# Optimization experiments

Hardware: AMD Instinct MI355X
Metric: run time of the kernel (lower is better)

## Reference

```python
import jax, jax.numpy as jnp
import numpy as np

N = 10000
E = 320000
IN_DIM = 256
OUT_DIM = 64
ALPHA = 0.2          # LeakyReLU negative slope
NEG_FILL = -9e15     # mask value used by the original module


def setup_inputs() -> dict:
    key = jax.random.key(0)
    k1, k2, k3, k4, k5 = jax.random.split(key, 5)
    X = jax.random.normal(k1, (N, IN_DIM), dtype=jnp.float32)
    edges = jnp.stack([
        jax.random.randint(k2, (E,), 0, N, dtype=jnp.int64 if jax.config.jax_enable_x64 else jnp.int32),
        jax.random.randint(k3, (E,), 0, N, dtype=jnp.int64 if jax.config.jax_enable_x64 else jnp.int32),
    ], axis=0)
    # Xavier-uniform-like init scales (gain 1.414)
    wlim = 1.414 * np.sqrt(6.0 / (IN_DIM + OUT_DIM))
    alim = 1.414 * np.sqrt(6.0 / (2 * OUT_DIM + 1))
    W = jax.random.uniform(k4, (IN_DIM, OUT_DIM), minval=-wlim, maxval=wlim, dtype=jnp.float32)
    a = jax.random.uniform(k5, (2 * OUT_DIM, 1), minval=-alim, maxval=alim, dtype=jnp.float32)
    return {"X": X, "edges": edges, "W": W, "a": a}


def reference(X, edges, W, a):
    # dropout p=0.0 -> identity in both dropout layers
    Wh = X @ W                                   # [N, F_out]
    src, dst = edges[0], edges[1]
    # per-edge attention logit: leakyrelu([Wh_src || Wh_dst] @ a)
    # split a to avoid materializing the concatenated [E, 2F] tensor
    a_src, a_dst = a[:OUT_DIM, 0], a[OUT_DIM:, 0]
    e = (Wh @ a_src)[src] + (Wh @ a_dst)[dst]    # [E]
    e = jnp.where(e > 0, e, ALPHA * e)           # LeakyReLU
    # dense N x N masked attention, exactly as the original module
    att = jnp.full((N, N), NEG_FILL, dtype=Wh.dtype)
    att = att.at[src, dst].set(e)
    att = jax.nn.softmax(att, axis=1)            # row-wise softmax
    h_prime = att @ Wh                           # [N, F_out]
    return h_prime
```

## Files before the change

### kernel.cpp

```cpp
#include <hip/hip_runtime.h>

#define N_NODES 10000
#define IN_DIM  256
#define OUT_DIM 64
#define ALPHA   0.2f
#define CAPS    128
#define NBG     625

typedef __attribute__((ext_vector_type(8))) short short8v;
typedef __attribute__((ext_vector_type(4))) float f32x4;

__device__ __forceinline__ ushort f2bf(float f) {
    unsigned u = __float_as_uint(f);
    return (ushort)((u + 0x7FFFu + ((u >> 16) & 1u)) >> 16);
}
__device__ __forceinline__ float bf2f(ushort u) {
    return __uint_as_float((unsigned)u << 16);
}

__global__ __launch_bounds__(256) void k_prep(const float* __restrict__ W,
                                              int* __restrict__ cur,
                                              ushort* __restrict__ Wf) {
    const int gid = blockIdx.x * 256 + threadIdx.x;
    for (int i = gid; i < N_NODES; i += 10240) cur[i] = 0;
    for (int w = gid; w < IN_DIM * OUT_DIM; w += 10240) {
        int k = w >> 6, c = w & 63;
        int s = k >> 5, k5 = k & 31, g = k5 >> 3, j = k5 & 7;
        int ct = c >> 4, li = c & 15;
        Wf[(((s * 4 + ct) * 64) + (g * 16 + li)) * 8 + j] = f2bf(W[w]);
    }
}

__global__ __launch_bounds__(256) void k_fused(const float* __restrict__ X,
                                               const ushort* __restrict__ Wf,
                                               const float* __restrict__ a,
                                               const int* __restrict__ src,
                                               const int* __restrict__ dst,
                                               int E,
                                               ushort* __restrict__ Whb,
                                               float* __restrict__ es,
                                               float* __restrict__ ed,
                                               int* __restrict__ cur,
                                               int* __restrict__ slots) {
    const int t = threadIdx.x;
    const int b = blockIdx.x;

    if (b >= NBG) {
        int i0 = (b - NBG) * 512 + t;
#pragma unroll
        for (int u = 0; u < 2; ++u) {
            int i = i0 + u * 256;
            if (i < E) {
                int s = src[i], d = dst[i];
                int p = atomicAdd(&cur[s], 1);
                if (p < CAPS) slots[(size_t)s * CAPS + p] = d;
            }
        }
        return;
    }

    __shared__ float les[16], led[16];
    if (t < 16) { les[t] = 0.f; led[t] = 0.f; }
    __syncthreads();

    const int wave = t >> 6;
    const int lane = t & 63;
    const int g = lane >> 4, li = lane & 15;
    const int row0 = b * 16;
    const float* __restrict__ xrow = X + (size_t)(row0 + li) * IN_DIM + g * 8;
    const short8v* __restrict__ Wfrag = (const short8v*)Wf;

    f32x4 acc = {0.f, 0.f, 0.f, 0.f};
#pragma unroll
    for (int s = 0; s < 8; ++s) {
        float4 xa = *(const float4*)(xrow + s * 32);
        float4 xb = *(const float4*)(xrow + s * 32 + 4);
        short8v af;
        af[0] = (short)f2bf(xa.x); af[1] = (short)f2bf(xa.y);
        af[2] = (short)f2bf(xa.z); af[3] = (short)f2bf(xa.w);
        af[4] = (short)f2bf(xb.x); af[5] = (short)f2bf(xb.y);
        af[6] = (short)f2bf(xb.z); af[7] = (short)f2bf(xb.w);
        short8v bfv = Wfrag[(s * 4 + wave) * 64 + lane];
        acc = __builtin_amdgcn_mfma_f32_16x16x32_bf16(af, bfv, acc, 0, 0, 0);
    }

    const int colC = wave * 16 + li;
    const float asrc = a[colC];
    const float adst = a[OUT_DIM + colC];
#pragma unroll
    for (int j = 0; j < 4; ++j) {
        int row = row0 + g * 4 + j;
        float v = acc[j];
        Whb[(size_t)row * OUT_DIM + colC] = f2bf(v);
        float se = v * asrc, sd = v * adst;
        se += __shfl_xor(se, 1, 64); sd += __shfl_xor(sd, 1, 64);
        se += __shfl_xor(se, 2, 64); sd += __shfl_xor(sd, 2, 64);
        se += __shfl_xor(se, 4, 64); sd += __shfl_xor(sd, 4, 64);
        se += __shfl_xor(se, 8, 64); sd += __shfl_xor(sd, 8, 64);
        if (li == 0) {
            atomicAdd(&les[g * 4 + j], se);
            atomicAdd(&led[g * 4 + j], sd);
        }
    }
    __syncthreads();
    if (t < 16) { es[row0 + t] = les[t]; ed[row0 + t] = led[t]; }
}

__global__ __launch_bounds__(64) void k_attn_slots(const int* __restrict__ cur,
                                                   const int* __restrict__ slots,
                                                   const float* __restrict__ es,
                                                   const float* __restrict__ ed,
                                                   const ushort* __restrict__ Whb,
                                                   float* __restrict__ out) {
    const int r = blockIdx.x;
    const int lane = threadIdx.x;
    int deg = cur[r];
    if (deg > CAPS) deg = CAPS;

    if (deg == 0) {
        float acc = 0.f;
        for (int j = 0; j < N_NODES; ++j) acc += bf2f(Whb[(size_t)j * OUT_DIM + lane]);
        out[(size_t)r * OUT_DIM + lane] = acc / (float)N_NODES;
        return;
    }

    __shared__ int   htab[256];
    __shared__ int   sdst[CAPS];
    __shared__ float sp[CAPS];

    for (int i = lane; i < 256; i += 64) htab[i] = -1;
    __syncthreads();

    const float er = es[r];

    float m = -INFINITY;
    for (int i = lane; i < deg; i += 64) {
        int d = slots[(size_t)r * CAPS + i];
        float e = er + ed[d];
        e = e > 0.f ? e : ALPHA * e;
        bool first = true;
        unsigned h = ((unsigned)d * 2654435761u) >> 24;
        while (true) {
            int prev = atomicCAS(&htab[h], -1, d);
            if (prev == -1) break;
            if (prev == d) { first = false; break; }
            h = (h + 1) & 255;
        }
        if (!first) e = -INFINITY;
        sdst[i] = d;
        sp[i] = e;
        m = fmaxf(m, e);
    }
#pragma unroll
    for (int o = 32; o > 0; o >>= 1) m = fmaxf(m, __shfl_xor(m, o, 64));
    __syncthreads();

    float ssum = 0.f;
    for (int i = lane; i < deg; i += 64) {
        float p = __expf(sp[i] - m);
        sp[i] = p;
        ssum += p;
    }
#pragma unroll
    for (int o = 32; o > 0; o >>= 1) ssum += __shfl_xor(ssum, o, 64);
    __syncthreads();

    const int h2 = lane >> 5;
    const int c  = lane & 31;
    const ushort2* __restrict__ W2 = (const ushort2*)Whb;
    float ax = 0.f, ay = 0.f;
    const int npairs = deg >> 1;
    int ip = 0;
    for (; ip + 8 <= npairs; ip += 8) {
        float p[8]; int q[8]; ushort2 w[8];
#pragma unroll
        for (int u = 0; u < 8; ++u) {
            int i = 2 * (ip + u) + h2;
            p[u] = sp[i]; q[u] = sdst[i];
        }
#pragma unroll
        for (int u = 0; u < 8; ++u) w[u] = W2[(size_t)q[u] * 32 + c];
#pragma unroll
        for (int u = 0; u < 8; ++u) {
            ax = fmaf(p[u], bf2f(w[u].x), ax);
            ay = fmaf(p[u], bf2f(w[u].y), ay);
        }
    }
    for (; ip < npairs; ++ip) {
        int i = 2 * ip + h2;
        float p = sp[i];
        ushort2 w = W2[(size_t)sdst[i] * 32 + c];
        ax = fmaf(p, bf2f(w.x), ax);
        ay = fmaf(p, bf2f(w.y), ay);
    }
    if ((deg & 1) && h2 == 0) {
        int i = deg - 1;
        float p = sp[i];
        ushort2 w = W2[(size_t)sdst[i] * 32 + c];
        ax = fmaf(p, bf2f(w.x), ax);
        ay = fmaf(p, bf2f(w.y), ay);
    }
    ax += __shfl_xor(ax, 32, 64);
    ay += __shfl_xor(ay, 32, 64);
    if (h2 == 0) {
        float inv = 1.f / ssum;
        ((float2*)out)[(size_t)r * 32 + c] = make_float2(ax * inv, ay * inv);
    }
}

__global__ __launch_bounds__(256) void k_gemm_mfma(const float* __restrict__ X,
                                                   const float* __restrict__ W,
                                                   const float* __restrict__ a,
                                                   ushort* __restrict__ Whb,
                                                   float* __restrict__ es,
                                                   float* __restrict__ ed,
                                                   int* __restrict__ zero10k) {
    const int t = threadIdx.x;
    const int b = blockIdx.x;
    const int gid = b * 256 + t;
    if (gid < N_NODES) zero10k[gid] = 0;

    __shared__ short8v bfragv[8 * 4 * 64];
    __shared__ float les[16], led[16];
    for (int w = t; w < IN_DIM * OUT_DIM; w += 256) {
        int k = w >> 6, c = w & 63;
        int s = k >> 5, k5 = k & 31, g = k5 >> 3, j = k5 & 7;
        int ct = c >> 4, li = c & 15;
        ((ushort*)bfragv)[(((s * 4 + ct) * 64) + (g * 16 + li)) * 8 + j] = f2bf(W[w]);
    }
    if (t < 16) { les[t] = 0.f; led[t] = 0.f; }
    __syncthreads();

    const int wave = t >> 6, lane = t & 63;
    const int g = lane >> 4, li = lane & 15;
    const int row0 = b * 16;
    const float* __restrict__ xrow = X + (size_t)(row0 + li) * IN_DIM + g * 8;

    f32x4 acc = {0.f, 0.f, 0.f, 0.f};
#pragma unroll
    for (int s = 0; s < 8; ++s) {
        float4 xa = *(const float4*)(xrow + s * 32);
        float4 xb = *(const float4*)(xrow + s * 32 + 4);
        short8v af;
        af[0] = (short)f2bf(xa.x); af[1] = (short)f2bf(xa.y);
        af[2] = (short)f2bf(xa.z); af[3] = (short)f2bf(xa.w);
        af[4] = (short)f2bf(xb.x); af[5] = (short)f2bf(xb.y);
        af[6] = (short)f2bf(xb.z); af[7] = (short)f2bf(xb.w);
        short8v bfv = bfragv[(s * 4 + wave) * 64 + lane];
        acc = __builtin_amdgcn_mfma_f32_16x16x32_bf16(af, bfv, acc, 0, 0, 0);
    }
    const int colC = wave * 16 + li;
    const float asrc = a[colC];
    const float adst = a[OUT_DIM + colC];
#pragma unroll
    for (int j = 0; j < 4; ++j) {
        int row = row0 + g * 4 + j;
        float v = acc[j];
        Whb[(size_t)row * OUT_DIM + colC] = f2bf(v);
        float se = v * asrc, sd = v * adst;
        se += __shfl_xor(se, 1, 64); sd += __shfl_xor(sd, 1, 64);
        se += __shfl_xor(se, 2, 64); sd += __shfl_xor(sd, 2, 64);
        se += __shfl_xor(se, 4, 64); sd += __shfl_xor(sd, 4, 64);
        se += __shfl_xor(se, 8, 64); sd += __shfl_xor(sd, 8, 64);
        if (li == 0) { atomicAdd(&les[g * 4 + j], se); atomicAdd(&led[g * 4 + j], sd); }
    }
    __syncthreads();
    if (t < 16) { es[row0 + t] = les[t]; ed[row0 + t] = led[t]; }
}

__global__ void k_fill_slots(const int* __restrict__ src, const int* __restrict__ dst,
                             int E, int* __restrict__ cur, int* __restrict__ slots) {
    int i = blockIdx.x * 256 + threadIdx.x;
    if (i < E) {
        int s = src[i], d = dst[i];
        int p = atomicAdd(&cur[s], 1);
        if (p < CAPS) slots[(size_t)s * CAPS + p] = d;
    }
}

extern "C" void kernel_launch(void* const* d_in, const int* in_sizes, int n_in,
                              void* d_out, int out_size, void* d_ws, size_t ws_size,
                              hipStream_t stream) {
    const float* X     = (const float*)d_in[0];
    const int*   edges = (const int*)d_in[1];
    const float* W     = (const float*)d_in[2];
    const float* a     = (const float*)d_in[3];
    float* out = (float*)d_out;

    const int E = in_sizes[1] / 2;
    const int* src = edges;
    const int* dst = edges + E;

    char* ws = (char*)d_ws;
    size_t o = 0;
    auto carve = [&](size_t bytes) -> void* {
        o = (o + 255) & ~(size_t)255;
        void* p = ws + o;
        o += bytes;
        return p;
    };
    ushort* Whb   = (ushort*)carve((size_t)N_NODES * OUT_DIM * 2);
    float*  es    = (float*)carve((size_t)N_NODES * 4);
    float*  ed    = (float*)carve((size_t)N_NODES * 4);
    int*    cur   = (int*)carve((size_t)N_NODES * 4);
    int*    slots = (int*)carve((size_t)N_NODES * CAPS * 4);
    ushort* Wf    = (ushort*)carve((size_t)IN_DIM * OUT_DIM * 2);

    const int nsc = (E + 511) / 512;

    if (o <= ws_size) {
        k_prep      <<<40, 256, 0, stream>>>(W, cur, Wf);
        k_fused     <<<NBG + nsc, 256, 0, stream>>>(X, Wf, a, src, dst, E,
                                                    Whb, es, ed, cur, slots);
        k_attn_slots<<<N_NODES, 64, 0, stream>>>(cur, slots, es, ed, Whb, out);
    } else {
        k_gemm_mfma <<<NBG, 256, 0, stream>>>(X, W, a, Whb, es, ed, cur);
        k_fill_slots<<<(E + 255) / 256, 256, 0, stream>>>(src, dst, E, cur, slots);
        k_attn_slots<<<N_NODES, 64, 0, stream>>>(cur, slots, es, ed, Whb, out);
    }
}
```

Measured before the change: 44.78 us.

## Deduplicate edges via global per-row hash table during scatter

Replaces the per-row append counter and the later shared-memory dedup hash with an open-addressed hash table per source row in global memory, filled with atomicCAS during edge scatter. The attention kernel then reads all 128 slots directly, compacts the valid entries with ballots and computes the softmax in registers without loops or a per-row hash pass. This requires initialising the full 5 MB slot array to -1 in the prep kernel, instead of zeroing only the 10k counters. Probing with global atomicCAS can also cost more under collisions. The fallback path for small workspaces is removed.

```diff
diff --git a/kernel.cpp b/kernel.cpp
--- a/kernel.cpp
+++ b/kernel.cpp
@@ -19,11 +19,12 @@
 }
 
 __global__ __launch_bounds__(256) void k_prep(const float* __restrict__ W,
-                                              int* __restrict__ cur,
+                                              int4* __restrict__ slots4,
                                               ushort* __restrict__ Wf) {
     const int gid = blockIdx.x * 256 + threadIdx.x;
-    for (int i = gid; i < N_NODES; i += 10240) cur[i] = 0;
-    for (int w = gid; w < IN_DIM * OUT_DIM; w += 10240) {
+    const int4 neg = make_int4(-1, -1, -1, -1);
+    for (int i = gid; i < N_NODES * CAPS / 4; i += 65536) slots4[i] = neg;
+    for (int w = gid; w < IN_DIM * OUT_DIM; w += 65536) {
         int k = w >> 6, c = w & 63;
         int s = k >> 5, k5 = k & 31, g = k5 >> 3, j = k5 & 7;
         int ct = c >> 4, li = c & 15;
@@ -40,7 +41,6 @@
                                                ushort* __restrict__ Whb,
                                                float* __restrict__ es,
                                                float* __restrict__ ed,
-                                               int* __restrict__ cur,
                                                int* __restrict__ slots) {
     const int t = threadIdx.x;
     const int b = blockIdx.x;
@@ -52,8 +52,13 @@
             int i = i0 + u * 256;
             if (i < E) {
                 int s = src[i], d = dst[i];
-                int p = atomicAdd(&cur[s], 1);
-                if (p < CAPS) slots[(size_t)s * CAPS + p] = d;
+                int* row = slots + (size_t)s * CAPS;
+                unsigned h = ((unsigned)d * 2654435761u) >> 25;
+                for (int it = 0; it < CAPS; ++it) {
+                    int prev = atomicCAS(&row[h], -1, d);
+                    if (prev == -1 || prev == d) break;
+                    h = (h + 1) & (CAPS - 1);
+                }
             }
         }
         return;
@@ -106,70 +111,63 @@
     if (t < 16) { es[row0 + t] = les[t]; ed[row0 + t] = led[t]; }
 }
 
-__global__ __launch_bounds__(64) void k_attn_slots(const int* __restrict__ cur,
-                                                   const int* __restrict__ slots,
-                                                   const float* __restrict__ es,
-                                                   const float* __restrict__ ed,
-                                                   const ushort* __restrict__ Whb,
-                                                   float* __restrict__ out) {
+__global__ __launch_bounds__(64) void k_attn_hash(const int* __restrict__ slots,
+                                                  const float* __restrict__ es,
+                                                  const float* __restrict__ ed,
+                                                  const ushort* __restrict__ Whb,
+                                                  float* __restrict__ out) {
     const int r = blockIdx.x;
     const int lane = threadIdx.x;
-    int deg = cur[r];
-    if (deg > CAPS) deg = CAPS;
-
-    if (deg == 0) {
+
+    int d0 = slots[(size_t)r * CAPS + lane];
+    int d1 = slots[(size_t)r * CAPS + 64 + lane];
+    const bool v0 = d0 >= 0, v1 = d1 >= 0;
+    const unsigned long long mask0 = __ballot(v0);
+    const unsigned long long mask1 = __ballot(v1);
+
+    if ((mask0 | mask1) == 0ull) {
         float acc = 0.f;
         for (int j = 0; j < N_NODES; ++j) acc += bf2f(Whb[(size_t)j * OUT_DIM + lane]);
         out[(size_t)r * OUT_DIM + lane] = acc / (float)N_NODES;
         return;
     }
 
-    __shared__ int   htab[256];
+    const float er = es[r];
+    float t0 = er + ed[v0 ? d0 : 0];  t0 = t0 > 0.f ? t0 : ALPHA * t0;
+    float t1 = er + ed[v1 ? d1 : 0];  t1 = t1 > 0.f ? t1 : ALPHA * t1;
+    float e0 = v0 ? t0 : -INFINITY;
+    float e1 = v1 ? t1 : -INFINITY;
+
+    float m = fmaxf(e0, e1);
+#pragma unroll
+    for (int o = 32; o > 0; o >>= 1) m = fmaxf(m, __shfl_xor(m, o, 64));
+
+    float p0 = v0 ? __expf(e0 - m) : 0.f;
+    float p1 = v1 ? __expf(e1 - m) : 0.f;
+    float ssum = p0 + p1;
+#pragma unroll
+    for (int o = 32; o > 0; o >>= 1) ssum += __shfl_xor(ssum, o, 64);
+
     __shared__ int   sdst[CAPS];
     __shared__ float sp[CAPS];
-
-    for (int i = lane; i < 256; i += 64) htab[i] = -1;
-    __syncthreads();
-
-    const float er = es[r];
-
-    float m = -INFINITY;
-    for (int i = lane; i < deg; i += 64) {
-        int d = slots[(size_t)r * CAPS + i];
-        float e = er + ed[d];
-        e = e > 0.f ? e : ALPHA * e;
-        bool first = true;
-        unsigned h = ((unsigned)d * 2654435761u) >> 24;
-        while (true) {
-            int prev = atomicCAS(&htab[h], -1, d);
-            if (prev == -1) break;
-            if (prev == d) { first = false; break; }
-            h = (h + 1) & 255;
-        }
-        if (!first) e = -INFINITY;
-        sdst[i] = d;
-        sp[i] = e;
-        m = fmaxf(m, e);
-    }
-#pragma unroll
-    for (int o = 32; o > 0; o >>= 1) m = fmaxf(m, __shfl_xor(m, o, 64));
-    __syncthreads();
-
-    float ssum = 0.f;
-    for (int i = lane; i < deg; i += 64) {
-        float p = __expf(sp[i] - m);
-        sp[i] = p;
-        ssum += p;
-    }
-#pragma unroll
-    for (int o = 32; o > 0; o >>= 1) ssum += __shfl_xor(ssum, o, 64);
+    const unsigned long long below = (1ull << lane) - 1ull;
+    const int cnt0 = __popcll(mask0);
+    if (v0) {
+        int p = __popcll(mask0 & below);
+        sdst[p] = d0; sp[p] = p0;
+    }
+    if (v1) {
+        int p = cnt0 + __popcll(mask1 & below);
+        sdst[p] = d1; sp[p] = p1;
+    }
+    const int count = cnt0 + __popcll(mask1);
     __syncthreads();
 
     const int h2 = lane >> 5;
     const int c  = lane & 31;
     const ushort2* __restrict__ W2 = (const ushort2*)Whb;
     float ax = 0.f, ay = 0.f;
-    const int npairs = deg >> 1;
+    const int npairs = count >> 1;
     int ip = 0;
     for (; ip + 8 <= npairs; ip += 8) {
         float p[8]; int q[8]; ushort2 w[8];
@@ -193,8 +191,8 @@
         ax = fmaf(p, bf2f(w.x), ax);
         ay = fmaf(p, bf2f(w.y), ay);
     }
-    if ((deg & 1) && h2 == 0) {
-        int i = deg - 1;
+    if ((count & 1) && h2 == 0) {
+        int i = count - 1;
         float p = sp[i];
         ushort2 w = W2[(size_t)sdst[i] * 32 + c];
         ax = fmaf(p, bf2f(w.x), ax);
@@ -205,76 +203,6 @@
     if (h2 == 0) {
         float inv = 1.f / ssum;
         ((float2*)out)[(size_t)r * 32 + c] = make_float2(ax * inv, ay * inv);
-    }
-}
-
-__global__ __launch_bounds__(256) void k_gemm_mfma(const float* __restrict__ X,
-                                                   const float* __restrict__ W,
-                                                   const float* __restrict__ a,
-                                                   ushort* __restrict__ Whb,
-                                                   float* __restrict__ es,
-                                                   float* __restrict__ ed,
-                                                   int* __restrict__ zero10k) {
-    const int t = threadIdx.x;
-    const int b = blockIdx.x;
-    const int gid = b * 256 + t;
-    if (gid < N_NODES) zero10k[gid] = 0;
-
-    __shared__ short8v bfragv[8 * 4 * 64];
-    __shared__ float les[16], led[16];
-    for (int w = t; w < IN_DIM * OUT_DIM; w += 256) {
-        int k = w >> 6, c = w & 63;
-        int s = k >> 5, k5 = k & 31, g = k5 >> 3, j = k5 & 7;
-        int ct = c >> 4, li = c & 15;
-        ((ushort*)bfragv)[(((s * 4 + ct) * 64) + (g * 16 + li)) * 8 + j] = f2bf(W[w]);
-    }
-    if (t < 16) { les[t] = 0.f; led[t] = 0.f; }
-    __syncthreads();
-
-    const int wave = t >> 6, lane = t & 63;
-    const int g = lane >> 4, li = lane & 15;
-    const int row0 = b * 16;
-    const float* __restrict__ xrow = X + (size_t)(row0 + li) * IN_DIM + g * 8;
-
-    f32x4 acc = {0.f, 0.f, 0.f, 0.f};
-#pragma unroll
-    for (int s = 0; s < 8; ++s) {
-        float4 xa = *(const float4*)(xrow + s * 32);
-        float4 xb = *(const float4*)(xrow + s * 32 + 4);
-        short8v af;
-        af[0] = (short)f2bf(xa.x); af[1] = (short)f2bf(xa.y);
-        af[2] = (short)f2bf(xa.z); af[3] = (short)f2bf(xa.w);
-        af[4] = (short)f2bf(xb.x); af[5] = (short)f2bf(xb.y);
-        af[6] = (short)f2bf(xb.z); af[7] = (short)f2bf(xb.w);
-        short8v bfv = bfragv[(s * 4 + wave) * 64 + lane];
-        acc = __builtin_amdgcn_mfma_f32_16x16x32_bf16(af, bfv, acc, 0, 0, 0);
-    }
-    const int colC = wave * 16 + li;
-    const float asrc = a[colC];
-    const float adst = a[OUT_DIM + colC];
-#pragma unroll
-    for (int j = 0; j < 4; ++j) {
-        int row = row0 + g * 4 + j;
-        float v = acc[j];
-        Whb[(size_t)row * OUT_DIM + colC] = f2bf(v);
-        float se = v * asrc, sd = v * adst;
-        se += __shfl_xor(se, 1, 64); sd += __shfl_xor(sd, 1, 64);
-        se += __shfl_xor(se, 2, 64); sd += __shfl_xor(sd, 2, 64);
-        se += __shfl_xor(se, 4, 64); sd += __shfl_xor(sd, 4, 64);
-        se += __shfl_xor(se, 8, 64); sd += __shfl_xor(sd, 8, 64);
-        if (li == 0) { atomicAdd(&les[g * 4 + j], se); atomicAdd(&led[g * 4 + j], sd); }
-    }
-    __syncthreads();
-    if (t < 16) { es[row0 + t] = les[t]; ed[row0 + t] = led[t]; }
-}
-
-__global__ void k_fill_slots(const int* __restrict__ src, const int* __restrict__ dst,
-                             int E, int* __restrict__ cur, int* __restrict__ slots) {
-    int i = blockIdx.x * 256 + threadIdx.x;
-    if (i < E) {
-        int s = src[i], d = dst[i];
-        int p = atomicAdd(&cur[s], 1);
-        if (p < CAPS) slots[(size_t)s * CAPS + p] = d;
     }
 }
 
@@ -302,20 +230,13 @@
     ushort* Whb   = (ushort*)carve((size_t)N_NODES * OUT_DIM * 2);
     float*  es    = (float*)carve((size_t)N_NODES * 4);
     float*  ed    = (float*)carve((size_t)N_NODES * 4);
-    int*    cur   = (int*)carve((size_t)N_NODES * 4);
     int*    slots = (int*)carve((size_t)N_NODES * CAPS * 4);
     ushort* Wf    = (ushort*)carve((size_t)IN_DIM * OUT_DIM * 2);
 
     const int nsc = (E + 511) / 512;
 
-    if (o <= ws_size) {
-        k_prep      <<<40, 256, 0, stream>>>(W, cur, Wf);
-        k_fused     <<<NBG + nsc, 256, 0, stream>>>(X, Wf, a, src, dst, E,
-                                                    Whb, es, ed, cur, slots);
-        k_attn_slots<<<N_NODES, 64, 0, stream>>>(cur, slots, es, ed, Whb, out);
-    } else {
-        k_gemm_mfma <<<NBG, 256, 0, stream>>>(X, W, a, Whb, es, ed, cur);
-        k_fill_slots<<<(E + 255) / 256, 256, 0, stream>>>(src, dst, E, cur, slots);
-        k_attn_slots<<<N_NODES, 64, 0, stream>>>(cur, slots, es, ed, Whb, out);
-    }
-}
+    k_prep     <<<256, 256, 0, stream>>>(W, (int4*)slots, Wf);
+    k_fused    <<<NBG + nsc, 256, 0, stream>>>(X, Wf, a, src, dst, E,
+                                               Whb, es, ed, slots);
+    k_attn_hash<<<N_NODES, 64, 0, stream>>>(slots, es, ed, Whb, out);
+}
```

New measurement: 42.27 us. -5.6%, faster.
